# Performance work log

Hardware: AMD Instinct MI355X
Metric: run time of the kernel (lower is better)

The kernel has to match this reference:

```python
import jax, jax.numpy as jnp
from jax import lax
import numpy as np

GROUPS = 128
EPS = 1e-7


def setup_inputs() -> dict:
    key = jax.random.key(0)
    k1, k2, k3, k4 = jax.random.split(key, 4)
    B, Cin, Cout, H, W, K = 8, 256, 256, 128, 128, 3
    return {
        "x": jax.random.normal(k1, (B, Cin, H, W), jnp.float32),
        "dw_kernels": jax.random.normal(k2, (B, Cout, Cin // GROUPS, K, K), jnp.float32) * 0.1,
        "pw_kernels": jax.random.normal(k3, (B, Cout, Cout // GROUPS, 1, 1), jnp.float32) * 0.1,
        "biases": jax.random.normal(k4, (B, Cout), jnp.float32) * 0.1,
    }


def _normalize(x):
    # torch.std uses Bessel's correction (divide by N-1)
    mean = jnp.mean(x, axis=(2, 3), keepdims=True)
    n = x.shape[2] * x.shape[3]
    var = jnp.sum((x - mean) ** 2, axis=(2, 3), keepdims=True) / (n - 1)
    std = jnp.sqrt(var) + EPS
    return (x - mean) / std


def _adaconv(x, dw_kernels, pw_kernels, biases):
    B, Cin, H, W = x.shape
    Cout = dw_kernels.shape[1]
    K = dw_kernels.shape[-1]
    pad = (K - 1) // 2

    xn = _normalize(x)
    xp = jnp.pad(xn, ((0, 0), (0, 0), (pad, pad), (pad, pad)))

    # per-sample grouped spatial conv via vmap over batch
    def dw_one(xi, wi):
        # xi: [Cin, H+2p, W+2p], wi: [Cout, Cin//G, K, K]
        return lax.conv_general_dilated(
            xi[None], wi, window_strides=(1, 1), padding="VALID",
            feature_group_count=GROUPS)[0]

    dw_out = jax.vmap(dw_one)(xp, dw_kernels)  # [B, Cout, H, W]

    # grouped 1x1 conv as a per-group small matmul
    cg = Cout // GROUPS
    dwg = dw_out.reshape(B, GROUPS, cg, H, W)
    pwg = pw_kernels.reshape(B, GROUPS, cg, cg)  # [b, g, out_sub, in_sub]
    out = jnp.einsum("bgoi,bgihw->bgohw", pwg, dwg).reshape(B, Cout, H, W)
    return out + biases[:, :, None, None]


def reference(x, dw_kernels, pw_kernels, biases):
    return _adaconv(x, dw_kernels, pw_kernels, biases)
```

## Files before the change

### kernel.cpp

```cpp
#include <hip/hip_runtime.h>
#include <math.h>

#define BATCH 8
#define CH    256
#define HH    128
#define WW    128
#define HW    (HH*WW)
#define NGRP  128
#define CPG   2
#define EPS   1e-7f

__global__ __launch_bounds__(256) void stats_kernel(
    const float* __restrict__ x, float* __restrict__ mean_o, float* __restrict__ rstd_o)
{
    const int c = blockIdx.x;
    const float4* p = (const float4*)(x + (size_t)c * HW);
    float s = 0.f, ss = 0.f;
    #pragma unroll 4
    for (int i = threadIdx.x; i < HW/4; i += 256) {
        float4 v = p[i];
        s  += v.x + v.y + v.z + v.w;
        ss += v.x*v.x + v.y*v.y + v.z*v.z + v.w*v.w;
    }
    #pragma unroll
    for (int off = 32; off > 0; off >>= 1) {
        s  += __shfl_down(s,  off);
        ss += __shfl_down(ss, off);
    }
    __shared__ float ls[4], lss[4];
    const int wave = threadIdx.x >> 6;
    if ((threadIdx.x & 63) == 0) { ls[wave] = s; lss[wave] = ss; }
    __syncthreads();
    if (threadIdx.x == 0) {
        s  = ls[0]  + ls[1]  + ls[2]  + ls[3];
        ss = lss[0] + lss[1] + lss[2] + lss[3];
        const float m = s * (1.0f / (float)HW);
        float var = (ss - s * m) * (1.0f / (float)(HW - 1));
        var = fmaxf(var, 0.0f);
        const float sd = sqrtf(var) + EPS;
        mean_o[c] = m;
        rstd_o[c] = 1.0f / sd;
    }
}

#define TH 16
#define XSS 136

__global__ __launch_bounds__(256) void adaconv_kernel(
    const float* __restrict__ x,
    const float* __restrict__ dwk,
    const float* __restrict__ pwk,
    const float* __restrict__ bias,
    const float* __restrict__ mean_i,
    const float* __restrict__ rstd_i,
    float* __restrict__ out)
{
    const int b   = blockIdx.z;
    const int g   = blockIdx.y;
    const int th0 = blockIdx.x * TH;
    const int bc0 = b * CH + g * CPG;
    const int tid = threadIdx.x;

    __shared__ float xs[CPG][TH + 2][XSS];

    const float r0s = rstd_i[bc0],     m0 = mean_i[bc0];
    const float r1s = rstd_i[bc0 + 1], m1 = mean_i[bc0 + 1];
    const float nm0 = -m0 * r0s, nm1 = -m1 * r1s;
    const float* xb = x + (size_t)bc0 * HW;

    if (tid < CPG * (TH + 2)) {
        const int ci  = tid / (TH + 2);
        const int row = tid - ci * (TH + 2);
        xs[ci][row][3]   = 0.f;
        xs[ci][row][132] = 0.f;
    }

    for (int e = tid; e < CPG * (TH + 2) * 32; e += 256) {
        const int ci  = e / ((TH + 2) * 32);
        const int rem = e - ci * ((TH + 2) * 32);
        const int row = rem >> 5;
        const int c4  = rem & 31;
        const int gh  = th0 + row - 1;
        float4 v = make_float4(0.f, 0.f, 0.f, 0.f);
        if (gh >= 0 && gh < HH) {
            v = *(const float4*)(xb + (size_t)ci * HW + gh * WW + (c4 << 2));
            const float sc = ci ? r1s : r0s;
            const float ad = ci ? nm1 : nm0;
            v.x = fmaf(v.x, sc, ad); v.y = fmaf(v.y, sc, ad);
            v.z = fmaf(v.z, sc, ad); v.w = fmaf(v.w, sc, ad);
        }
        *(float4*)&xs[ci][row][4 + (c4 << 2)] = v;
    }

    const float p00 = pwk[(size_t)(bc0 + 0) * 2 + 0];
    const float p01 = pwk[(size_t)(bc0 + 0) * 2 + 1];
    const float p10 = pwk[(size_t)(bc0 + 1) * 2 + 0];
    const float p11 = pwk[(size_t)(bc0 + 1) * 2 + 1];
    const float* dwb = dwk + (size_t)bc0 * 18;
    float we[2][2][9];
    #pragma unroll
    for (int ci = 0; ci < 2; ++ci)
        #pragma unroll
        for (int k = 0; k < 9; ++k) {
            const float w0 = dwb[ci * 9 + k];
            const float w1 = dwb[18 + ci * 9 + k];
            we[0][ci][k] = fmaf(p00, w0, p01 * w1);
            we[1][ci][k] = fmaf(p10, w0, p11 * w1);
        }
    const float bb0 = bias[bc0], bb1 = bias[bc0 + 1];

    __syncthreads();

    const int c0    = (tid & 31) << 2;
    const int rbase = (tid >> 5) << 1;

    float acc[2][2][4];
    #pragma unroll
    for (int o = 0; o < 2; ++o)
        #pragma unroll
        for (int cc = 0; cc < 4; ++cc) { acc[o][0][cc] = bb0; acc[o][1][cc] = bb1; }

    #pragma unroll
    for (int r = 0; r < 4; ++r) {
        #pragma unroll
        for (int ci = 0; ci < 2; ++ci) {
            const float* rowp = &xs[ci][rbase + r][0];
            const float2 L = *(const float2*)(rowp + c0 + 2);
            const float4 M = *(const float4*)(rowp + c0 + 4);
            const float2 R = *(const float2*)(rowp + c0 + 8);
            const float xv[6] = { L.y, M.x, M.y, M.z, M.w, R.x };
            #pragma unroll
            for (int o = 0; o < 2; ++o) {
                const int ky = r - o;
                if (ky < 0 || ky > 2) continue;
                #pragma unroll
                for (int ch = 0; ch < 2; ++ch)
                    #pragma unroll
                    for (int cc = 0; cc < 4; ++cc)
                        #pragma unroll
                        for (int kx = 0; kx < 3; ++kx)
                            acc[o][ch][cc] = fmaf(we[ch][ci][ky * 3 + kx],
                                                  xv[cc + kx], acc[o][ch][cc]);
            }
        }
    }

    float* outb = out + (size_t)bc0 * HW;
    #pragma unroll
    for (int o = 0; o < 2; ++o) {
        const int gr = th0 + rbase + o;
        #pragma unroll
        for (int ch = 0; ch < 2; ++ch) {
            const float4 vv = make_float4(acc[o][ch][0], acc[o][ch][1],
                                          acc[o][ch][2], acc[o][ch][3]);
            *(float4*)(outb + (size_t)ch * HW + gr * WW + c0) = vv;
        }
    }
}

extern "C" void kernel_launch(void* const* d_in, const int* in_sizes, int n_in,
                              void* d_out, int out_size, void* d_ws, size_t ws_size,
                              hipStream_t stream)
{
    const float* x    = (const float*)d_in[0];
    const float* dwk  = (const float*)d_in[1];
    const float* pwk  = (const float*)d_in[2];
    const float* bias = (const float*)d_in[3];
    float* out = (float*)d_out;

    float* mean_b = (float*)d_ws;
    float* rstd_b = mean_b + BATCH * CH;

    stats_kernel<<<BATCH * CH, 256, 0, stream>>>(x, mean_b, rstd_b);

    dim3 grid(HH / TH, NGRP, BATCH);
    adaconv_kernel<<<grid, 256, 0, stream>>>(x, dwk, pwk, bias, mean_b, rstd_b, out);
}
```

Measured before the change: 274.8 us.

## Fuse channel statistics into conv kernel with whole-plane shared memory tile

Replaces the separate stats pass and row-tiled conv with one kernel per (batch, group) that loads both full 128x128 channel planes into LDS, computing sum and sum-of-squares during the load. Normalization is folded into the effective weights and bias, and the halo is padded with the mean so raw values can be used directly. This removes the second global read of x and one kernel launch. In exchange each block uses about 141 KB of LDS, which permits only one block per CU, and the grid shrinks to 1024 blocks, so latency hiding may suffer.

```diff
diff --git a/kernel.cpp b/kernel.cpp
--- a/kernel.cpp
+++ b/kernel.cpp
@@ -7,153 +7,149 @@
 #define WW    128
 #define HW    (HH*WW)
 #define NGRP  128
-#define CPG   2
 #define EPS   1e-7f
+#define XSS   136
 
-__global__ __launch_bounds__(256) void stats_kernel(
-    const float* __restrict__ x, float* __restrict__ mean_o, float* __restrict__ rstd_o)
-{
-    const int c = blockIdx.x;
-    const float4* p = (const float4*)(x + (size_t)c * HW);
-    float s = 0.f, ss = 0.f;
-    #pragma unroll 4
-    for (int i = threadIdx.x; i < HW/4; i += 256) {
-        float4 v = p[i];
-        s  += v.x + v.y + v.z + v.w;
-        ss += v.x*v.x + v.y*v.y + v.z*v.z + v.w*v.w;
-    }
-    #pragma unroll
-    for (int off = 32; off > 0; off >>= 1) {
-        s  += __shfl_down(s,  off);
-        ss += __shfl_down(ss, off);
-    }
-    __shared__ float ls[4], lss[4];
-    const int wave = threadIdx.x >> 6;
-    if ((threadIdx.x & 63) == 0) { ls[wave] = s; lss[wave] = ss; }
-    __syncthreads();
-    if (threadIdx.x == 0) {
-        s  = ls[0]  + ls[1]  + ls[2]  + ls[3];
-        ss = lss[0] + lss[1] + lss[2] + lss[3];
-        const float m = s * (1.0f / (float)HW);
-        float var = (ss - s * m) * (1.0f / (float)(HW - 1));
-        var = fmaxf(var, 0.0f);
-        const float sd = sqrtf(var) + EPS;
-        mean_o[c] = m;
-        rstd_o[c] = 1.0f / sd;
-    }
-}
-
-#define TH 16
-#define XSS 136
-
-__global__ __launch_bounds__(256) void adaconv_kernel(
+__global__ __launch_bounds__(512) void fused_adaconv_kernel(
     const float* __restrict__ x,
     const float* __restrict__ dwk,
     const float* __restrict__ pwk,
     const float* __restrict__ bias,
-    const float* __restrict__ mean_i,
-    const float* __restrict__ rstd_i,
     float* __restrict__ out)
 {
-    const int b   = blockIdx.z;
-    const int g   = blockIdx.y;
-    const int th0 = blockIdx.x * TH;
-    const int bc0 = b * CH + g * CPG;
+    const int g   = blockIdx.x;
+    const int b   = blockIdx.y;
+    const int bc0 = b * CH + g * 2;
     const int tid = threadIdx.x;
 
-    __shared__ float xs[CPG][TH + 2][XSS];
+    __shared__ float xs[2][HH + 2][XSS];
+    __shared__ float red[16];
+    __shared__ float stat[4];
 
-    const float r0s = rstd_i[bc0],     m0 = mean_i[bc0];
-    const float r1s = rstd_i[bc0 + 1], m1 = mean_i[bc0 + 1];
-    const float nm0 = -m0 * r0s, nm1 = -m1 * r1s;
     const float* xb = x + (size_t)bc0 * HW;
 
-    if (tid < CPG * (TH + 2)) {
-        const int ci  = tid / (TH + 2);
-        const int row = tid - ci * (TH + 2);
-        xs[ci][row][3]   = 0.f;
-        xs[ci][row][132] = 0.f;
+    const int ci = tid >> 8;
+    const int tl = tid & 255;
+    const float4* src = (const float4*)(xb + (size_t)ci * HW);
+    float s = 0.f, ss = 0.f;
+    #pragma unroll
+    for (int k = 0; k < 16; ++k) {
+        const int f = (k << 8) + tl;
+        float4 v = src[f];
+        s  += v.x + v.y + v.z + v.w;
+        ss += v.x*v.x + v.y*v.y + v.z*v.z + v.w*v.w;
+        *(float4*)&xs[ci][(f >> 5) + 1][4 + ((f & 31) << 2)] = v;
     }
 
-    for (int e = tid; e < CPG * (TH + 2) * 32; e += 256) {
-        const int ci  = e / ((TH + 2) * 32);
-        const int rem = e - ci * ((TH + 2) * 32);
-        const int row = rem >> 5;
-        const int c4  = rem & 31;
-        const int gh  = th0 + row - 1;
-        float4 v = make_float4(0.f, 0.f, 0.f, 0.f);
-        if (gh >= 0 && gh < HH) {
-            v = *(const float4*)(xb + (size_t)ci * HW + gh * WW + (c4 << 2));
-            const float sc = ci ? r1s : r0s;
-            const float ad = ci ? nm1 : nm0;
-            v.x = fmaf(v.x, sc, ad); v.y = fmaf(v.y, sc, ad);
-            v.z = fmaf(v.z, sc, ad); v.w = fmaf(v.w, sc, ad);
-        }
-        *(float4*)&xs[ci][row][4 + (c4 << 2)] = v;
+    #pragma unroll
+    for (int off = 32; off; off >>= 1) {
+        s  += __shfl_down(s,  off);
+        ss += __shfl_down(ss, off);
     }
+    const int wv = tid >> 6;
+    if ((tid & 63) == 0) { red[wv] = s; red[8 + wv] = ss; }
+    __syncthreads();
+    if (tid < 2) {
+        const int base = tid * 4;
+        const float S  = red[base] + red[base+1] + red[base+2] + red[base+3];
+        const float SS = red[8+base] + red[9+base] + red[10+base] + red[11+base];
+        const float m  = S * (1.0f / (float)HW);
+        float var = (SS - S * m) * (1.0f / (float)(HW - 1));
+        var = fmaxf(var, 0.0f);
+        stat[tid * 2]     = m;
+        stat[tid * 2 + 1] = 1.0f / (sqrtf(var) + EPS);
+    }
+    __syncthreads();
+    const float m0 = stat[0], r0 = stat[1], m1 = stat[2], r1 = stat[3];
 
-    const float p00 = pwk[(size_t)(bc0 + 0) * 2 + 0];
-    const float p01 = pwk[(size_t)(bc0 + 0) * 2 + 1];
-    const float p10 = pwk[(size_t)(bc0 + 1) * 2 + 0];
-    const float p11 = pwk[(size_t)(bc0 + 1) * 2 + 1];
-    const float* dwb = dwk + (size_t)bc0 * 18;
-    float we[2][2][9];
-    #pragma unroll
-    for (int ci = 0; ci < 2; ++ci)
-        #pragma unroll
-        for (int k = 0; k < 9; ++k) {
-            const float w0 = dwb[ci * 9 + k];
-            const float w1 = dwb[18 + ci * 9 + k];
-            we[0][ci][k] = fmaf(p00, w0, p01 * w1);
-            we[1][ci][k] = fmaf(p10, w0, p11 * w1);
-        }
-    const float bb0 = bias[bc0], bb1 = bias[bc0 + 1];
-
-    __syncthreads();
-
-    const int c0    = (tid & 31) << 2;
-    const int rbase = (tid >> 5) << 1;
-
-    float acc[2][2][4];
-    #pragma unroll
-    for (int o = 0; o < 2; ++o)
-        #pragma unroll
-        for (int cc = 0; cc < 4; ++cc) { acc[o][0][cc] = bb0; acc[o][1][cc] = bb1; }
-
-    #pragma unroll
-    for (int r = 0; r < 4; ++r) {
-        #pragma unroll
-        for (int ci = 0; ci < 2; ++ci) {
-            const float* rowp = &xs[ci][rbase + r][0];
-            const float2 L = *(const float2*)(rowp + c0 + 2);
-            const float4 M = *(const float4*)(rowp + c0 + 4);
-            const float2 R = *(const float2*)(rowp + c0 + 8);
-            const float xv[6] = { L.y, M.x, M.y, M.z, M.w, R.x };
-            #pragma unroll
-            for (int o = 0; o < 2; ++o) {
-                const int ky = r - o;
-                if (ky < 0 || ky > 2) continue;
-                #pragma unroll
-                for (int ch = 0; ch < 2; ++ch)
-                    #pragma unroll
-                    for (int cc = 0; cc < 4; ++cc)
-                        #pragma unroll
-                        for (int kx = 0; kx < 3; ++kx)
-                            acc[o][ch][cc] = fmaf(we[ch][ci][ky * 3 + kx],
-                                                  xv[cc + kx], acc[o][ch][cc]);
-            }
+    for (int e = tid; e < 1056; e += 512) {
+        const int c  = (e >= 528);
+        const int i  = c ? (e - 528) : e;
+        const float mv = c ? m1 : m0;
+        if (i < 272) {
+            const int row = (i < 136) ? 0 : (HH + 1);
+            const int col = (i < 136) ? i : (i - 136);
+            xs[c][row][col] = mv;
+        } else {
+            const int r2  = i - 272;
+            const int row = 1 + (r2 & 127);
+            const int col = (r2 < 128) ? 3 : 132;
+            xs[c][row][col] = mv;
         }
     }
 
+    const float p00 = pwk[(size_t)bc0 * 2 + 0];
+    const float p01 = pwk[(size_t)bc0 * 2 + 1];
+    const float p10 = pwk[(size_t)bc0 * 2 + 2];
+    const float p11 = pwk[(size_t)bc0 * 2 + 3];
+    const float* dwb = dwk + (size_t)bc0 * 18;
+    float we[2][2][9];
+    float bb[2] = { bias[bc0], bias[bc0 + 1] };
+    #pragma unroll
+    for (int cc = 0; cc < 2; ++cc) {
+        const float rr = cc ? r1 : r0;
+        const float mm = cc ? m1 : m0;
+        #pragma unroll
+        for (int k = 0; k < 9; ++k) {
+            const float w0 = dwb[cc * 9 + k];
+            const float w1 = dwb[18 + cc * 9 + k];
+            const float e0 = fmaf(p00, w0, p01 * w1) * rr;
+            const float e1 = fmaf(p10, w0, p11 * w1) * rr;
+            we[0][cc][k] = e0;
+            we[1][cc][k] = e1;
+            bb[0] -= mm * e0;
+            bb[1] -= mm * e1;
+        }
+    }
+    __syncthreads();
+
+    const int c0  = (tid & 31) << 2;
+    const int rb0 = (tid >> 5) << 3;
     float* outb = out + (size_t)bc0 * HW;
+
     #pragma unroll
-    for (int o = 0; o < 2; ++o) {
-        const int gr = th0 + rbase + o;
+    for (int hc = 0; hc < 2; ++hc) {
+        const int rb = rb0 + hc * 4;
+        float acc[4][2][4];
         #pragma unroll
-        for (int ch = 0; ch < 2; ++ch) {
-            const float4 vv = make_float4(acc[o][ch][0], acc[o][ch][1],
-                                          acc[o][ch][2], acc[o][ch][3]);
-            *(float4*)(outb + (size_t)ch * HW + gr * WW + c0) = vv;
+        for (int j = 0; j < 4; ++j)
+            #pragma unroll
+            for (int q = 0; q < 4; ++q) { acc[j][0][q] = bb[0]; acc[j][1][q] = bb[1]; }
+
+        #pragma unroll
+        for (int xr = 0; xr < 6; ++xr) {
+            #pragma unroll
+            for (int cin = 0; cin < 2; ++cin) {
+                const float* rowp = &xs[cin][rb + xr][0];
+                const float2 L = *(const float2*)(rowp + c0 + 2);
+                const float4 M = *(const float4*)(rowp + c0 + 4);
+                const float2 R = *(const float2*)(rowp + c0 + 8);
+                const float xv[6] = { L.y, M.x, M.y, M.z, M.w, R.x };
+                #pragma unroll
+                for (int j = 0; j < 4; ++j) {
+                    const int ky = xr - j;
+                    if (ky < 0 || ky > 2) continue;
+                    #pragma unroll
+                    for (int ch = 0; ch < 2; ++ch)
+                        #pragma unroll
+                        for (int q = 0; q < 4; ++q)
+                            #pragma unroll
+                            for (int kx = 0; kx < 3; ++kx)
+                                acc[j][ch][q] = fmaf(we[ch][cin][ky * 3 + kx],
+                                                     xv[q + kx], acc[j][ch][q]);
+                }
+            }
+        }
+
+        #pragma unroll
+        for (int j = 0; j < 4; ++j) {
+            const int gr = rb + j;
+            #pragma unroll
+            for (int ch = 0; ch < 2; ++ch) {
+                const float4 vv = make_float4(acc[j][ch][0], acc[j][ch][1],
+                                              acc[j][ch][2], acc[j][ch][3]);
+                *(float4*)(outb + (size_t)ch * HW + gr * WW + c0) = vv;
+            }
         }
     }
 }
@@ -168,11 +164,6 @@
     const float* bias = (const float*)d_in[3];
     float* out = (float*)d_out;
 
-    float* mean_b = (float*)d_ws;
-    float* rstd_b = mean_b + BATCH * CH;
-
-    stats_kernel<<<BATCH * CH, 256, 0, stream>>>(x, mean_b, rstd_b);
-
-    dim3 grid(HH / TH, NGRP, BATCH);
-    adaconv_kernel<<<grid, 256, 0, stream>>>(x, dwk, pwk, bias, mean_b, rstd_b, out);
+    dim3 grid(NGRP, BATCH);
+    fused_adaconv_kernel<<<grid, 512, 0, stream>>>(x, dwk, pwk, bias, out);
 }
```

After: 251.7 us. -8.4%, faster.

## Fold normalization into conv weights and double rows per thread

Applied to the files above, without the earlier changes.

Folds the per-channel normalization into the fused depthwise and pointwise weights and the bias. Halo padding is filled with the channel mean, so raw x is staged into shared memory without a per-element FMA. The row tile grows from 16 to 32, so each thread computes 4 output rows instead of 2, which cuts halo reloads and shared-memory reads per output. It also sets a launch-bounds occupancy hint of 4; the larger accumulator array raises register pressure, and folding the mean into the bias can add cancellation error in fp32.

```diff
diff --git a/kernel.cpp b/kernel.cpp
--- a/kernel.cpp
+++ b/kernel.cpp
@@ -7,7 +7,6 @@
 #define WW    128
 #define HW    (HH*WW)
 #define NGRP  128
-#define CPG   2
 #define EPS   1e-7f
 
 __global__ __launch_bounds__(256) void stats_kernel(
@@ -37,16 +36,15 @@
         const float m = s * (1.0f / (float)HW);
         float var = (ss - s * m) * (1.0f / (float)(HW - 1));
         var = fmaxf(var, 0.0f);
-        const float sd = sqrtf(var) + EPS;
         mean_o[c] = m;
-        rstd_o[c] = 1.0f / sd;
+        rstd_o[c] = 1.0f / (sqrtf(var) + EPS);
     }
 }
 
-#define TH 16
+#define TH  32
 #define XSS 136
 
-__global__ __launch_bounds__(256) void adaconv_kernel(
+__global__ __launch_bounds__(256, 4) void conv_kernel(
     const float* __restrict__ x,
     const float* __restrict__ dwk,
     const float* __restrict__ pwk,
@@ -55,104 +53,106 @@
     const float* __restrict__ rstd_i,
     float* __restrict__ out)
 {
+    const int gh0 = blockIdx.x * TH;
+    const int g   = blockIdx.y;
     const int b   = blockIdx.z;
-    const int g   = blockIdx.y;
-    const int th0 = blockIdx.x * TH;
-    const int bc0 = b * CH + g * CPG;
+    const int bc0 = b * CH + g * 2;
     const int tid = threadIdx.x;
 
-    __shared__ float xs[CPG][TH + 2][XSS];
+    __shared__ float xs[2][TH + 2][XSS];
 
-    const float r0s = rstd_i[bc0],     m0 = mean_i[bc0];
-    const float r1s = rstd_i[bc0 + 1], m1 = mean_i[bc0 + 1];
-    const float nm0 = -m0 * r0s, nm1 = -m1 * r1s;
+    const float m0 = mean_i[bc0],     r0 = rstd_i[bc0];
+    const float m1 = mean_i[bc0 + 1], r1 = rstd_i[bc0 + 1];
     const float* xb = x + (size_t)bc0 * HW;
 
-    if (tid < CPG * (TH + 2)) {
-        const int ci  = tid / (TH + 2);
-        const int row = tid - ci * (TH + 2);
-        xs[ci][row][3]   = 0.f;
-        xs[ci][row][132] = 0.f;
-    }
-
-    for (int e = tid; e < CPG * (TH + 2) * 32; e += 256) {
+    for (int e = tid; e < 2 * (TH + 2) * 32; e += 256) {
         const int ci  = e / ((TH + 2) * 32);
         const int rem = e - ci * ((TH + 2) * 32);
         const int row = rem >> 5;
         const int c4  = rem & 31;
-        const int gh  = th0 + row - 1;
-        float4 v = make_float4(0.f, 0.f, 0.f, 0.f);
-        if (gh >= 0 && gh < HH) {
+        const int gh  = gh0 + row - 1;
+        const float mv = ci ? m1 : m0;
+        float4 v = make_float4(mv, mv, mv, mv);
+        if (gh >= 0 && gh < HH)
             v = *(const float4*)(xb + (size_t)ci * HW + gh * WW + (c4 << 2));
-            const float sc = ci ? r1s : r0s;
-            const float ad = ci ? nm1 : nm0;
-            v.x = fmaf(v.x, sc, ad); v.y = fmaf(v.y, sc, ad);
-            v.z = fmaf(v.z, sc, ad); v.w = fmaf(v.w, sc, ad);
-        }
         *(float4*)&xs[ci][row][4 + (c4 << 2)] = v;
     }
+    if (tid < 2 * (TH + 2)) {
+        const int ci  = tid / (TH + 2);
+        const int row = tid - ci * (TH + 2);
+        const float mv = ci ? m1 : m0;
+        xs[ci][row][3]   = mv;
+        xs[ci][row][132] = mv;
+        xs[ci][row][133] = mv;
+    }
 
-    const float p00 = pwk[(size_t)(bc0 + 0) * 2 + 0];
-    const float p01 = pwk[(size_t)(bc0 + 0) * 2 + 1];
-    const float p10 = pwk[(size_t)(bc0 + 1) * 2 + 0];
-    const float p11 = pwk[(size_t)(bc0 + 1) * 2 + 1];
+    const float p00 = pwk[(size_t)bc0 * 2 + 0];
+    const float p01 = pwk[(size_t)bc0 * 2 + 1];
+    const float p10 = pwk[(size_t)bc0 * 2 + 2];
+    const float p11 = pwk[(size_t)bc0 * 2 + 3];
     const float* dwb = dwk + (size_t)bc0 * 18;
     float we[2][2][9];
+    float bb[2] = { bias[bc0], bias[bc0 + 1] };
     #pragma unroll
-    for (int ci = 0; ci < 2; ++ci)
+    for (int cin = 0; cin < 2; ++cin) {
+        const float rr = cin ? r1 : r0;
+        const float mm = cin ? m1 : m0;
         #pragma unroll
         for (int k = 0; k < 9; ++k) {
-            const float w0 = dwb[ci * 9 + k];
-            const float w1 = dwb[18 + ci * 9 + k];
-            we[0][ci][k] = fmaf(p00, w0, p01 * w1);
-            we[1][ci][k] = fmaf(p10, w0, p11 * w1);
+            const float w0 = dwb[cin * 9 + k];
+            const float w1 = dwb[18 + cin * 9 + k];
+            const float e0 = fmaf(p00, w0, p01 * w1) * rr;
+            const float e1 = fmaf(p10, w0, p11 * w1) * rr;
+            we[0][cin][k] = e0;
+            we[1][cin][k] = e1;
+            bb[0] -= mm * e0;
+            bb[1] -= mm * e1;
         }
-    const float bb0 = bias[bc0], bb1 = bias[bc0 + 1];
-
+    }
     __syncthreads();
 
-    const int c0    = (tid & 31) << 2;
-    const int rbase = (tid >> 5) << 1;
+    const int c0 = (tid & 31) << 2;
+    const int rb = (tid >> 5) << 2;
 
-    float acc[2][2][4];
+    float acc[4][2][4];
     #pragma unroll
-    for (int o = 0; o < 2; ++o)
+    for (int j = 0; j < 4; ++j)
         #pragma unroll
-        for (int cc = 0; cc < 4; ++cc) { acc[o][0][cc] = bb0; acc[o][1][cc] = bb1; }
+        for (int q = 0; q < 4; ++q) { acc[j][0][q] = bb[0]; acc[j][1][q] = bb[1]; }
 
     #pragma unroll
-    for (int r = 0; r < 4; ++r) {
+    for (int xr = 0; xr < 6; ++xr) {
         #pragma unroll
-        for (int ci = 0; ci < 2; ++ci) {
-            const float* rowp = &xs[ci][rbase + r][0];
+        for (int cin = 0; cin < 2; ++cin) {
+            const float* rowp = &xs[cin][rb + xr][0];
             const float2 L = *(const float2*)(rowp + c0 + 2);
             const float4 M = *(const float4*)(rowp + c0 + 4);
             const float2 R = *(const float2*)(rowp + c0 + 8);
             const float xv[6] = { L.y, M.x, M.y, M.z, M.w, R.x };
             #pragma unroll
-            for (int o = 0; o < 2; ++o) {
-                const int ky = r - o;
+            for (int j = 0; j < 4; ++j) {
+                const int ky = xr - j;
                 if (ky < 0 || ky > 2) continue;
                 #pragma unroll
                 for (int ch = 0; ch < 2; ++ch)
                     #pragma unroll
-                    for (int cc = 0; cc < 4; ++cc)
+                    for (int q = 0; q < 4; ++q)
                         #pragma unroll
                         for (int kx = 0; kx < 3; ++kx)
-                            acc[o][ch][cc] = fmaf(we[ch][ci][ky * 3 + kx],
-                                                  xv[cc + kx], acc[o][ch][cc]);
+                            acc[j][ch][q] = fmaf(we[ch][cin][ky * 3 + kx],
+                                                 xv[q + kx], acc[j][ch][q]);
             }
         }
     }
 
     float* outb = out + (size_t)bc0 * HW;
     #pragma unroll
-    for (int o = 0; o < 2; ++o) {
-        const int gr = th0 + rbase + o;
+    for (int j = 0; j < 4; ++j) {
+        const int gr = gh0 + rb + j;
         #pragma unroll
         for (int ch = 0; ch < 2; ++ch) {
-            const float4 vv = make_float4(acc[o][ch][0], acc[o][ch][1],
-                                          acc[o][ch][2], acc[o][ch][3]);
+            const float4 vv = make_float4(acc[j][ch][0], acc[j][ch][1],
+                                          acc[j][ch][2], acc[j][ch][3]);
             *(float4*)(outb + (size_t)ch * HW + gr * WW + c0) = vv;
         }
     }
@@ -174,5 +174,5 @@
     stats_kernel<<<BATCH * CH, 256, 0, stream>>>(x, mean_b, rstd_b);
 
     dim3 grid(HH / TH, NGRP, BATCH);
-    adaconv_kernel<<<grid, 256, 0, stream>>>(x, dwk, pwk, bias, mean_b, rstd_b, out);
+    conv_kernel<<<grid, 256, 0, stream>>>(x, dwk, pwk, bias, mean_b, rstd_b, out);
 }
```

New measurement: 265.3 us. 3.4% less time.
